# Optimization experiments

Measured on AMD Instinct MI355X. Metric: run time of the kernel, lower is better.

## Reference

```python
import jax, jax.numpy as jnp
import numpy as np
from jax import lax

N_T, B, C_IN, H, W = 24, 2, 9, 32, 32   # n timesteps, batch, bands, tile HxW
N_FILTER, KM, N_CLASS, HID = 32, 16, 10, 128


def setup_inputs() -> dict:
    key = jax.random.key(0)
    ks = jax.random.split(key, 6)
    x = jax.random.normal(ks[0], (N_T, B, C_IN, H, W), jnp.float32)
    kernels = jax.random.normal(ks[1], (N_FILTER, KM, C_IN), jnp.float32)  # DTW filter kernels
    W1 = jax.random.normal(ks[2], (N_FILTER, HID), jnp.float32) * 0.1
    b1 = jnp.zeros((HID,), jnp.float32)
    W2 = jax.random.normal(ks[3], (HID, HID), jnp.float32) * 0.1
    b2 = jnp.zeros((HID,), jnp.float32)
    Wl = jax.random.normal(ks[4], (HID, N_CLASS), jnp.float32) * 0.1
    bl = jnp.zeros((N_CLASS,), jnp.float32)
    return {"x": x, "kernels": kernels, "W1": W1, "b1": b1, "W2": W2, "b2": b2, "Wl": Wl, "bl": bl}


def _dtw_single(kernel, seq):
    # kernel: (m, c), seq: (n, c). Classic DTW with squared-euclidean local cost,
    # then sum of local costs along the optimal alignment path (path is non-diff,
    # matching the torch code's detached dtw_path + differentiable squared diffs).
    C = jnp.sum((kernel[:, None, :] - seq[None, :, :]) ** 2, axis=-1)  # (m, n)
    m, n = C.shape
    inf = jnp.array(jnp.inf, C.dtype)
    row0 = jnp.cumsum(C[0])

    def row_step(prev, crow):
        prev_shift = jnp.concatenate([jnp.full((1,), inf, C.dtype), prev[:-1]])
        def col_step(left, cud):
            c, up, diag = cud
            d = c + jnp.minimum(left, jnp.minimum(up, diag))
            return d, d
        _, row = lax.scan(col_step, inf, (crow, prev, prev_shift))
        return row, row

    _, rows = lax.scan(row_step, row0, C[1:])
    D = lax.stop_gradient(jnp.concatenate([row0[None, :], rows], axis=0))  # (m, n)

    def bt_step(carry, _):
        i, j, acc, done = carry
        im1 = jnp.maximum(i - 1, 0)
        jm1 = jnp.maximum(j - 1, 0)
        cand = jnp.stack([
            jnp.where((i > 0) & (j > 0), D[im1, jm1], inf),  # diagonal
            jnp.where(i > 0, D[im1, j], inf),                # up
            jnp.where(j > 0, D[i, jm1], inf)])               # left
        choice = jnp.argmin(cand)  # first-min tie-break = diagonal preferred (as np.argmin)
        ni = jnp.where(choice == 2, i, im1)
        nj = jnp.where(choice == 1, j, jm1)
        ni = jnp.where(done, i, ni)
        nj = jnp.where(done, j, nj)
        acc = acc + jnp.where(done, jnp.array(0.0, C.dtype), C[ni, nj])
        done = done | ((ni == 0) & (nj == 0))
        return (ni, nj, acc, done), None

    init = (jnp.int32(m - 1), jnp.int32(n - 1), C[m - 1, n - 1], jnp.array(m == 1 and n == 1))
    (_, _, total, _), _ = lax.scan(bt_step, init, None, length=m + n - 2)
    return total


def reference(x, kernels, W1, b1, W2, b2, Wl, bl):
    n, b, c, h, w = x.shape
    # torch.cat(list_of_n, dim=0).view(-1, n, c) == row-major reshape of (n,b,c,h,w)
    seqs = x.reshape(-1, n, c)  # (B2, n, c), B2 = b*h*w
    feats = jax.vmap(lambda s: jax.vmap(lambda k: _dtw_single(k, s))(kernels))(seqs)  # (B2, F)
    t = jax.nn.relu(feats @ W1 + b1)
    t = jax.nn.relu(t @ W2 + b2)
    t = jax.nn.softmax(t @ Wl + bl, axis=1)
    return t.reshape(b, N_CLASS, h, w)
```

## Files before the change

kernel.cpp:

```cpp
#include <hip/hip_runtime.h>

#define NT   24
#define CIN  9
#define NF   32
#define KM   16
#define HID  128
#define NCLS 10
#define SEQ_LEN (NT*CIN)
#define PADJ 12
#define NSTRIP 4

__global__ __launch_bounds__(128, 4) void dtwnet_fused(
    const float* __restrict__ x,
    const float* __restrict__ kern,
    const float* __restrict__ W1, const float* __restrict__ b1,
    const float* __restrict__ W2, const float* __restrict__ b2,
    const float* __restrict__ Wl, const float* __restrict__ bl,
    float* __restrict__ out)
{
  __shared__ float seq_lds[NT*PADJ];
  __shared__ float feat_lds[NF];
  __shared__ float h1_lds[HID];
  __shared__ float h2_lds[HID];
  __shared__ float logit_lds[NCLS];

  const int tid  = threadIdx.x;
  const int bid  = blockIdx.x;
  const int wave = tid >> 6;
  const int lane = tid & 63;
  const int s    = lane >> 4;
  const int f_lo = lane & 15;
  const int f    = wave*16 + f_lo;

  for (int d = tid; d < SEQ_LEN; d += 128) {
    int jj = d / CIN, cc = d - jj*CIN;
    seq_lds[jj*PADJ + cc] = x[bid*SEQ_LEN + d];
  }
  __syncthreads();

  float kf[4*CIN];
  {
    const float4* kp = (const float4*)(kern + f*(KM*CIN) + s*(4*CIN));
    #pragma unroll
    for (int q = 0; q < 9; ++q) {
      float4 t4 = kp[q];
      kf[4*q+0]=t4.x; kf[4*q+1]=t4.y; kf[4*q+2]=t4.z; kf[4*q+3]=t4.w;
    }
  }

  float rowD[4], rowS[4];
  float bndUpD=0.f, bndUpS=0.f, bndDgD=0.f, bndDgS=0.f;

  #pragma unroll 1
  for (int t = 0; t < NT + NSTRIP - 1; ++t) {
    int j = t - s;
    bool active = (j >= 0) && (j < NT);
    float nbD = 0.f, nbS = 0.f;
    if (active) {
      const float4* sp = (const float4*)(seq_lds + j*PADJ);
      float4 q0 = sp[0], q1 = sp[1], q2 = sp[2];
      float sv[CIN] = {q0.x,q0.y,q0.z,q0.w,q1.x,q1.y,q1.z,q1.w,q2.x};
      float cost[4];
      #pragma unroll
      for (int r = 0; r < 4; ++r) {
        float cc = 0.f;
        #pragma unroll
        for (int c = 0; c < CIN; ++c) { float d = kf[r*CIN+c] - sv[c]; cc = fmaf(d, d, cc); }
        cost[r] = cc;
      }
      if (j == 0) {
        float accD = (s == 0) ? 0.f : bndUpD;
        float accS = (s == 0) ? 0.f : bndUpS;
        #pragma unroll
        for (int r = 0; r < 4; ++r) { accD += cost[r]; accS += cost[r]; rowD[r]=accD; rowS[r]=accS; }
      } else {
        float upD, upS, diagD, diagS;
        float leftD = rowD[0], leftS = rowS[0];
        float D0, S0;
        if (s == 0) {
          D0 = cost[0] + leftD; S0 = cost[0] + leftS;
        } else {
          float mn = fminf(bndDgD, fminf(bndUpD, leftD));
          D0 = cost[0] + mn;
          bool tD = (bndDgD <= bndUpD) && (bndDgD <= leftD);
          bool tU = (bndUpD <= leftD);
          S0 = cost[0] + (tD ? bndDgS : (tU ? bndUpS : leftS));
        }
        diagD = leftD; diagS = leftS;
        rowD[0] = D0; rowS[0] = S0; upD = D0; upS = S0;
        #pragma unroll
        for (int r = 1; r < 4; ++r) {
          float lD = rowD[r], lS = rowS[r];
          float mn = fminf(diagD, fminf(upD, lD));
          float D2 = cost[r] + mn;
          bool tD = (diagD <= upD) && (diagD <= lD);
          bool tU = (upD <= lD);
          float S2 = cost[r] + (tD ? diagS : (tU ? upS : lS));
          diagD = lD; diagS = lS;
          rowD[r] = D2; rowS[r] = S2; upD = D2; upS = S2;
        }
      }
      nbD = rowD[3]; nbS = rowS[3];
    }
    float rD = __shfl_up(nbD, 16u);
    float rS = __shfl_up(nbS, 16u);
    bndDgD = bndUpD; bndDgS = bndUpS;
    bndUpD = rD;     bndUpS = rS;
  }

  if (s == 3) feat_lds[f] = rowS[3];
  __syncthreads();

  {
    float acc = b1[tid];
    #pragma unroll
    for (int k = 0; k < NF; ++k) acc = fmaf(feat_lds[k], W1[k*HID + tid], acc);
    h1_lds[tid] = fmaxf(acc, 0.f);
  }
  __syncthreads();
  {
    const float4* hh = (const float4*)h1_lds;
    float a0 = b2[tid], a1 = 0.f, a2 = 0.f, a3 = 0.f;
    #pragma unroll
    for (int k = 0; k < HID/4; ++k) {
      float4 h4 = hh[k];
      a0 = fmaf(h4.x, W2[(4*k+0)*HID + tid], a0);
      a1 = fmaf(h4.y, W2[(4*k+1)*HID + tid], a1);
      a2 = fmaf(h4.z, W2[(4*k+2)*HID + tid], a2);
      a3 = fmaf(h4.w, W2[(4*k+3)*HID + tid], a3);
    }
    h2_lds[tid] = fmaxf((a0 + a1) + (a2 + a3), 0.f);
  }
  __syncthreads();
  if (tid < NCLS) {
    const float4* hh = (const float4*)h2_lds;
    float a0 = bl[tid], a1 = 0.f, a2 = 0.f, a3 = 0.f;
    #pragma unroll
    for (int k = 0; k < HID/4; ++k) {
      float4 h4 = hh[k];
      a0 = fmaf(h4.x, Wl[(4*k+0)*NCLS + tid], a0);
      a1 = fmaf(h4.y, Wl[(4*k+1)*NCLS + tid], a1);
      a2 = fmaf(h4.z, Wl[(4*k+2)*NCLS + tid], a2);
      a3 = fmaf(h4.w, Wl[(4*k+3)*NCLS + tid], a3);
    }
    logit_lds[tid] = (a0 + a1) + (a2 + a3);
  }
  __syncthreads();
  if (tid == 0) {
    float mx = logit_lds[0];
    #pragma unroll
    for (int j = 1; j < NCLS; ++j) mx = fmaxf(mx, logit_lds[j]);
    float e[NCLS]; float sum = 0.f;
    #pragma unroll
    for (int j = 0; j < NCLS; ++j) { e[j] = __expf(logit_lds[j] - mx); sum += e[j]; }
    float inv = 1.f / sum;
    float* op = out + bid*NCLS;
    #pragma unroll
    for (int j = 0; j < NCLS; ++j) op[j] = e[j] * inv;
  }
}

extern "C" void kernel_launch(void* const* d_in, const int* in_sizes, int n_in,
                              void* d_out, int out_size, void* d_ws, size_t ws_size,
                              hipStream_t stream) {
  const float* x    = (const float*)d_in[0];
  const float* kern = (const float*)d_in[1];
  const float* W1   = (const float*)d_in[2];
  const float* b1   = (const float*)d_in[3];
  const float* W2   = (const float*)d_in[4];
  const float* b2   = (const float*)d_in[5];
  const float* Wl   = (const float*)d_in[6];
  const float* bl   = (const float*)d_in[7];
  float* out = (float*)d_out;

  dtwnet_fused<<<2048, 128, 0, stream>>>(x, kern, W1, b1, W2, b2, Wl, bl, out);
}
```

Baseline: 89.98 us.

## Batch four sequences per block with packed two-filter DTW and expanded distance cost

Each block now handles four pixel sequences, one per wave, and each lane computes two DTW filters at once using packed float2 FMAs. The squared-distance cost is expanded as ||k||^2 + ||s||^2 - 2k·s, with the sequence norms precomputed in LDS. Separate path-sum tracking is dropped, since the DTW cumulative cost equals the path sum. The next sequence row is prefetched from LDS. The MLP layers are batched over the four sequences so each weight load is reused. The expanded cost can lose floating-point accuracy through cancellation, and the larger blocks change occupancy.

```diff
diff --git a/kernel.cpp b/kernel.cpp
--- a/kernel.cpp
+++ b/kernel.cpp
@@ -9,8 +9,11 @@
 #define SEQ_LEN (NT*CIN)
 #define PADJ 12
 #define NSTRIP 4
-
-__global__ __launch_bounds__(128, 4) void dtwnet_fused(
+#define SPB  4
+
+typedef float vf2 __attribute__((ext_vector_type(2)));
+
+__global__ __launch_bounds__(256, 2) void dtwnet_fused(
     const float* __restrict__ x,
     const float* __restrict__ kern,
     const float* __restrict__ W1, const float* __restrict__ b1,
@@ -18,143 +21,212 @@
     const float* __restrict__ Wl, const float* __restrict__ bl,
     float* __restrict__ out)
 {
-  __shared__ float seq_lds[NT*PADJ];
-  __shared__ float feat_lds[NF];
-  __shared__ float h1_lds[HID];
-  __shared__ float h2_lds[HID];
-  __shared__ float logit_lds[NCLS];
+  __shared__ float seq_lds[SPB*NT*PADJ];
+  __shared__ float feat_lds[SPB*NF];
+  __shared__ float h1_lds[SPB*HID];
+  __shared__ float h2_lds[SPB*HID];
+  __shared__ float logit_lds[SPB*NCLS];
 
   const int tid  = threadIdx.x;
   const int bid  = blockIdx.x;
   const int wave = tid >> 6;
   const int lane = tid & 63;
   const int s    = lane >> 4;
-  const int f_lo = lane & 15;
-  const int f    = wave*16 + f_lo;
-
-  for (int d = tid; d < SEQ_LEN; d += 128) {
-    int jj = d / CIN, cc = d - jj*CIN;
-    seq_lds[jj*PADJ + cc] = x[bid*SEQ_LEN + d];
-  }
-  __syncthreads();
-
-  float kf[4*CIN];
+  const int fp   = lane & 15;
+
+  float kA[4*CIN], kB[4*CIN];
   {
-    const float4* kp = (const float4*)(kern + f*(KM*CIN) + s*(4*CIN));
+    const float4* ka = (const float4*)(kern + fp*(KM*CIN) + s*(4*CIN));
+    const float4* kb = (const float4*)(kern + (fp+16)*(KM*CIN) + s*(4*CIN));
     #pragma unroll
     for (int q = 0; q < 9; ++q) {
-      float4 t4 = kp[q];
-      kf[4*q+0]=t4.x; kf[4*q+1]=t4.y; kf[4*q+2]=t4.z; kf[4*q+3]=t4.w;
-    }
-  }
-
-  float rowD[4], rowS[4];
-  float bndUpD=0.f, bndUpS=0.f, bndDgD=0.f, bndDgS=0.f;
+      float4 ta = ka[q], tb = kb[q];
+      kA[4*q+0]=ta.x; kA[4*q+1]=ta.y; kA[4*q+2]=ta.z; kA[4*q+3]=ta.w;
+      kB[4*q+0]=tb.x; kB[4*q+1]=tb.y; kB[4*q+2]=tb.z; kB[4*q+3]=tb.w;
+    }
+  }
+
+  for (int d = tid; d < SPB*SEQ_LEN; d += 256) {
+    int sq = d / SEQ_LEN;
+    int r  = d - sq*SEQ_LEN;
+    int jj = r / CIN, cc = r - jj*CIN;
+    seq_lds[sq*NT*PADJ + jj*PADJ + cc] = x[bid*(SPB*SEQ_LEN) + d];
+  }
+  __syncthreads();
+
+  if (tid < SPB*NT) {
+    int sq = tid / NT, j = tid - sq*NT;
+    float* base = seq_lds + sq*NT*PADJ + j*PADJ;
+    const float4* bp = (const float4*)base;
+    float4 q0 = bp[0], q1 = bp[1];
+    float v8 = base[8];
+    base[9] = q0.x*q0.x + q0.y*q0.y + q0.z*q0.z + q0.w*q0.w
+            + q1.x*q1.x + q1.y*q1.y + q1.z*q1.z + q1.w*q1.w
+            + v8*v8;
+  }
+
+  vf2 kfp[4*CIN], arp[4];
+  #pragma unroll
+  for (int r = 0; r < 4; ++r) arp[r] = (vf2){0.f, 0.f};
+  #pragma unroll
+  for (int idx = 0; idx < 4*CIN; ++idx) {
+    int r = idx / CIN;
+    vf2 v = {kA[idx], kB[idx]};
+    arp[r] = __builtin_elementwise_fma(v, v, arp[r]);
+    kfp[idx] = v * (-2.f);
+  }
+  __syncthreads();
+
+  const float4* spv = (const float4*)(seq_lds + wave*NT*PADJ);
+
+  float rDA[4], rDB[4];
+  float bUpA = 0.f, bDgA = 0.f, bUpB = 0.f, bDgB = 0.f;
+
+  float4 q0 = spv[0], q1 = spv[1], q2 = spv[2];
 
   #pragma unroll 1
   for (int t = 0; t < NT + NSTRIP - 1; ++t) {
     int j = t - s;
-    bool active = (j >= 0) && (j < NT);
-    float nbD = 0.f, nbS = 0.f;
-    if (active) {
-      const float4* sp = (const float4*)(seq_lds + j*PADJ);
-      float4 q0 = sp[0], q1 = sp[1], q2 = sp[2];
+    int jn = j + 1;
+    jn = (jn < 0) ? 0 : ((jn > NT-1) ? NT-1 : jn);
+    float4 m0 = spv[jn*3+0], m1 = spv[jn*3+1], m2 = spv[jn*3+2];
+
+    float nbA = 0.f, nbB = 0.f;
+    if (j >= 0 && j < NT) {
       float sv[CIN] = {q0.x,q0.y,q0.z,q0.w,q1.x,q1.y,q1.z,q1.w,q2.x};
-      float cost[4];
+      float bj = q2.y;
+      vf2 cst[4];
       #pragma unroll
       for (int r = 0; r < 4; ++r) {
-        float cc = 0.f;
+        vf2 cc = arp[r] + bj;
         #pragma unroll
-        for (int c = 0; c < CIN; ++c) { float d = kf[r*CIN+c] - sv[c]; cc = fmaf(d, d, cc); }
-        cost[r] = cc;
+        for (int c = 0; c < CIN; ++c) {
+          vf2 sc = {sv[c], sv[c]};
+          cc = __builtin_elementwise_fma(kfp[r*CIN+c], sc, cc);
+        }
+        cst[r] = cc;
       }
       if (j == 0) {
-        float accD = (s == 0) ? 0.f : bndUpD;
-        float accS = (s == 0) ? 0.f : bndUpS;
+        float aA = (s == 0) ? 0.f : bUpA;
+        float aB = (s == 0) ? 0.f : bUpB;
         #pragma unroll
-        for (int r = 0; r < 4; ++r) { accD += cost[r]; accS += cost[r]; rowD[r]=accD; rowS[r]=accS; }
+        for (int r = 0; r < 4; ++r) {
+          aA += cst[r].x; rDA[r] = aA;
+          aB += cst[r].y; rDB[r] = aB;
+        }
       } else {
-        float upD, upS, diagD, diagS;
-        float leftD = rowD[0], leftS = rowS[0];
-        float D0, S0;
-        if (s == 0) {
-          D0 = cost[0] + leftD; S0 = cost[0] + leftS;
-        } else {
-          float mn = fminf(bndDgD, fminf(bndUpD, leftD));
-          D0 = cost[0] + mn;
-          bool tD = (bndDgD <= bndUpD) && (bndDgD <= leftD);
-          bool tU = (bndUpD <= leftD);
-          S0 = cost[0] + (tD ? bndDgS : (tU ? bndUpS : leftS));
-        }
-        diagD = leftD; diagS = leftS;
-        rowD[0] = D0; rowS[0] = S0; upD = D0; upS = S0;
-        #pragma unroll
-        for (int r = 1; r < 4; ++r) {
-          float lD = rowD[r], lS = rowS[r];
-          float mn = fminf(diagD, fminf(upD, lD));
-          float D2 = cost[r] + mn;
-          bool tD = (diagD <= upD) && (diagD <= lD);
-          bool tU = (upD <= lD);
-          float S2 = cost[r] + (tD ? diagS : (tU ? upS : lS));
-          diagD = lD; diagS = lS;
-          rowD[r] = D2; rowS[r] = S2; upD = D2; upS = S2;
+        {
+          float l0 = rDA[0];
+          float D0 = (s == 0) ? (cst[0].x + l0)
+                              : (cst[0].x + fminf(bDgA, fminf(bUpA, l0)));
+          float dg = l0, up = D0; rDA[0] = D0;
+          #pragma unroll
+          for (int r = 1; r < 4; ++r) {
+            float l = rDA[r];
+            float D = cst[r].x + fminf(dg, fminf(up, l));
+            dg = l; rDA[r] = D; up = D;
+          }
+        }
+        {
+          float l0 = rDB[0];
+          float D0 = (s == 0) ? (cst[0].y + l0)
+                              : (cst[0].y + fminf(bDgB, fminf(bUpB, l0)));
+          float dg = l0, up = D0; rDB[0] = D0;
+          #pragma unroll
+          for (int r = 1; r < 4; ++r) {
+            float l = rDB[r];
+            float D = cst[r].y + fminf(dg, fminf(up, l));
+            dg = l; rDB[r] = D; up = D;
+          }
         }
       }
-      nbD = rowD[3]; nbS = rowS[3];
-    }
-    float rD = __shfl_up(nbD, 16u);
-    float rS = __shfl_up(nbS, 16u);
-    bndDgD = bndUpD; bndDgS = bndUpS;
-    bndUpD = rD;     bndUpS = rS;
-  }
-
-  if (s == 3) feat_lds[f] = rowS[3];
-  __syncthreads();
-
-  {
-    float acc = b1[tid];
-    #pragma unroll
-    for (int k = 0; k < NF; ++k) acc = fmaf(feat_lds[k], W1[k*HID + tid], acc);
-    h1_lds[tid] = fmaxf(acc, 0.f);
-  }
-  __syncthreads();
-  {
-    const float4* hh = (const float4*)h1_lds;
-    float a0 = b2[tid], a1 = 0.f, a2 = 0.f, a3 = 0.f;
+      nbA = rDA[3]; nbB = rDB[3];
+    }
+    float rA = __shfl_up(nbA, 16u);
+    float rB = __shfl_up(nbB, 16u);
+    bDgA = bUpA; bUpA = rA;
+    bDgB = bUpB; bUpB = rB;
+    q0 = m0; q1 = m1; q2 = m2;
+  }
+
+  if (s == NSTRIP-1) {
+    feat_lds[wave*NF + fp]      = rDA[3];
+    feat_lds[wave*NF + fp + 16] = rDB[3];
+  }
+  __syncthreads();
+
+  if (tid < HID) {
+    float a0 = b1[tid], a1 = a0, a2 = a0, a3 = a0;
+    #pragma unroll
+    for (int k = 0; k < NF; ++k) {
+      float w = W1[k*HID + tid];
+      a0 = fmaf(feat_lds[0*NF + k], w, a0);
+      a1 = fmaf(feat_lds[1*NF + k], w, a1);
+      a2 = fmaf(feat_lds[2*NF + k], w, a2);
+      a3 = fmaf(feat_lds[3*NF + k], w, a3);
+    }
+    h1_lds[0*HID + tid] = fmaxf(a0, 0.f);
+    h1_lds[1*HID + tid] = fmaxf(a1, 0.f);
+    h1_lds[2*HID + tid] = fmaxf(a2, 0.f);
+    h1_lds[3*HID + tid] = fmaxf(a3, 0.f);
+  }
+  __syncthreads();
+  if (tid < HID) {
+    const float4* h0 = (const float4*)(h1_lds + 0*HID);
+    const float4* h1v = (const float4*)(h1_lds + 1*HID);
+    const float4* h2v = (const float4*)(h1_lds + 2*HID);
+    const float4* h3v = (const float4*)(h1_lds + 3*HID);
+    float p0 = b2[tid], p1 = 0.f, p2 = 0.f, p3 = 0.f;
+    float q0_ = b2[tid], q1_ = 0.f, q2_ = 0.f, q3_ = 0.f;
+    float r0 = b2[tid], r1 = 0.f, r2 = 0.f, r3 = 0.f;
+    float s0 = b2[tid], s1 = 0.f, s2 = 0.f, s3 = 0.f;
+    #pragma unroll
+    for (int k = 0; k < HID/4; ++k) {
+      float w0 = W2[(4*k+0)*HID + tid];
+      float w1 = W2[(4*k+1)*HID + tid];
+      float w2 = W2[(4*k+2)*HID + tid];
+      float w3 = W2[(4*k+3)*HID + tid];
+      float4 ha = h0[k], hb = h1v[k], hc = h2v[k], hd = h3v[k];
+      p0 = fmaf(ha.x, w0, p0); p1 = fmaf(ha.y, w1, p1);
+      p2 = fmaf(ha.z, w2, p2); p3 = fmaf(ha.w, w3, p3);
+      q0_ = fmaf(hb.x, w0, q0_); q1_ = fmaf(hb.y, w1, q1_);
+      q2_ = fmaf(hb.z, w2, q2_); q3_ = fmaf(hb.w, w3, q3_);
+      r0 = fmaf(hc.x, w0, r0); r1 = fmaf(hc.y, w1, r1);
+      r2 = fmaf(hc.z, w2, r2); r3 = fmaf(hc.w, w3, r3);
+      s0 = fmaf(hd.x, w0, s0); s1 = fmaf(hd.y, w1, s1);
+      s2 = fmaf(hd.z, w2, s2); s3 = fmaf(hd.w, w3, s3);
+    }
+    h2_lds[0*HID + tid] = fmaxf((p0 + p1) + (p2 + p3), 0.f);
+    h2_lds[1*HID + tid] = fmaxf((q0_ + q1_) + (q2_ + q3_), 0.f);
+    h2_lds[2*HID + tid] = fmaxf((r0 + r1) + (r2 + r3), 0.f);
+    h2_lds[3*HID + tid] = fmaxf((s0 + s1) + (s2 + s3), 0.f);
+  }
+  __syncthreads();
+  if (tid < SPB*NCLS) {
+    int sq = tid / NCLS, j = tid - sq*NCLS;
+    const float4* hh = (const float4*)(h2_lds + sq*HID);
+    float a0 = bl[j], a1 = 0.f, a2 = 0.f, a3 = 0.f;
     #pragma unroll
     for (int k = 0; k < HID/4; ++k) {
       float4 h4 = hh[k];
-      a0 = fmaf(h4.x, W2[(4*k+0)*HID + tid], a0);
-      a1 = fmaf(h4.y, W2[(4*k+1)*HID + tid], a1);
-      a2 = fmaf(h4.z, W2[(4*k+2)*HID + tid], a2);
-      a3 = fmaf(h4.w, W2[(4*k+3)*HID + tid], a3);
-    }
-    h2_lds[tid] = fmaxf((a0 + a1) + (a2 + a3), 0.f);
-  }
-  __syncthreads();
-  if (tid < NCLS) {
-    const float4* hh = (const float4*)h2_lds;
-    float a0 = bl[tid], a1 = 0.f, a2 = 0.f, a3 = 0.f;
-    #pragma unroll
-    for (int k = 0; k < HID/4; ++k) {
-      float4 h4 = hh[k];
-      a0 = fmaf(h4.x, Wl[(4*k+0)*NCLS + tid], a0);
-      a1 = fmaf(h4.y, Wl[(4*k+1)*NCLS + tid], a1);
-      a2 = fmaf(h4.z, Wl[(4*k+2)*NCLS + tid], a2);
-      a3 = fmaf(h4.w, Wl[(4*k+3)*NCLS + tid], a3);
+      a0 = fmaf(h4.x, Wl[(4*k+0)*NCLS + j], a0);
+      a1 = fmaf(h4.y, Wl[(4*k+1)*NCLS + j], a1);
+      a2 = fmaf(h4.z, Wl[(4*k+2)*NCLS + j], a2);
+      a3 = fmaf(h4.w, Wl[(4*k+3)*NCLS + j], a3);
     }
     logit_lds[tid] = (a0 + a1) + (a2 + a3);
   }
   __syncthreads();
-  if (tid == 0) {
-    float mx = logit_lds[0];
-    #pragma unroll
-    for (int j = 1; j < NCLS; ++j) mx = fmaxf(mx, logit_lds[j]);
+  if (tid < SPB) {
+    const float* lg = &logit_lds[tid*NCLS];
+    float mx = lg[0];
+    #pragma unroll
+    for (int j = 1; j < NCLS; ++j) mx = fmaxf(mx, lg[j]);
     float e[NCLS]; float sum = 0.f;
     #pragma unroll
-    for (int j = 0; j < NCLS; ++j) { e[j] = __expf(logit_lds[j] - mx); sum += e[j]; }
+    for (int j = 0; j < NCLS; ++j) { e[j] = __expf(lg[j] - mx); sum += e[j]; }
     float inv = 1.f / sum;
-    float* op = out + bid*NCLS;
+    float* op = out + (bid*SPB + tid)*NCLS;
     #pragma unroll
     for (int j = 0; j < NCLS; ++j) op[j] = e[j] * inv;
   }
@@ -173,5 +245,5 @@
   const float* bl   = (const float*)d_in[7];
   float* out = (float*)d_out;
 
-  dtwnet_fused<<<2048, 128, 0, stream>>>(x, kern, W1, b1, W2, b2, Wl, bl, out);
+  dtwnet_fused<<<512, 256, 0, stream>>>(x, kern, W1, b1, W2, b2, Wl, bl, out);
 }
```

Result: faster. 85.67 us (-4.8%).
